# Kernel tuning notes

Hardware: AMD Instinct MI355X
Metric: run time of the kernel (lower is better)

Reference implementation:

```python
import jax, jax.numpy as jnp
import numpy as np

H, W, C_IN, C_OUT, N = 512, 512, 256, 256, 65536


def setup_inputs() -> dict:
    key = jax.random.key(0)
    k1, k2, k3, k4 = jax.random.split(key, 4)
    feature = jax.random.normal(k1, (1, C_IN, H, W), dtype=jnp.float32)
    weight = jax.random.normal(k2, (C_OUT, C_IN, 3, 3), dtype=jnp.float32) * 0.05
    # base sparse locations in the unpadded map; build 3x3 neighborhood indices
    # into the PADDED ([H+2, W+2]) map, exactly like F.pad + fancy indexing.
    base_h = jax.random.randint(k3, (N,), 0, H, dtype=jnp.int32)
    base_w = jax.random.randint(k4, (N,), 0, W, dtype=jnp.int32)
    dh = jnp.repeat(jnp.arange(3, dtype=jnp.int32), 3)  # [9]: 0,0,0,1,1,1,2,2,2
    dw = jnp.tile(jnp.arange(3, dtype=jnp.int32), 3)    # [9]: 0,1,2,0,1,2,...
    h_idx = base_h[None, :] + dh[:, None]  # [9, N], values in [0, H+1]
    w_idx = base_w[None, :] + dw[:, None]  # [9, N], values in [0, W+1]
    return {"feature": feature, "weight": weight, "h_idx": h_idx, "w_idx": w_idx}


def reference(feature, weight, h_idx, w_idx):
    # feature: [1, C, H, W]; weight: [Cout, C, 3, 3]; h_idx/w_idx: [9, N]
    C = feature.shape[1]
    out_ch = weight.shape[0]
    # F.pad(feature, [1,1,1,1])[0] -> [C, H+2, W+2]
    padded = jnp.pad(feature, ((0, 0), (0, 0), (1, 1), (1, 1)))[0]
    # gather 3x3 neighborhoods at sparse locations -> [C, 9, N]
    gathered = padded[:, h_idx, w_idx]
    # .view(9*C, -1): contiguous reshape gives row index c*9 + k
    g = gathered.reshape(C * 9, -1)  # [C*9, N]
    # kernel_d2s = weight.view(out, -1): row ordering c*9 + (kh*3+kw) matches
    k2d = weight.reshape(out_ch, -1)  # [Cout, C*9]
    return k2d @ g  # [Cout, N]
```

## Files before the change

### kernel.cpp

```cpp
#include <hip/hip_runtime.h>
#include <hip/hip_bf16.h>

#define HH 512
#define WW 512
#define CIN 256
#define COUT 256
#define NPTS 65536
#define PW 514
#define NPIX (PW * PW)
#define NKT 72

typedef __bf16 bf16x8 __attribute__((ext_vector_type(8)));
typedef float f32x16 __attribute__((ext_vector_type(16)));
typedef unsigned short us8 __attribute__((ext_vector_type(8)));

static __device__ __forceinline__ unsigned short f2bf(float f) {
  unsigned u = __builtin_bit_cast(unsigned, f);
  unsigned r = u + 0x7fffu + ((u >> 16) & 1u);
  return (unsigned short)(r >> 16);
}

static __device__ __forceinline__ void gload16(const void* g, void* l) {
  __builtin_amdgcn_global_load_lds(
      (const __attribute__((address_space(1))) unsigned int*)g,
      (__attribute__((address_space(3))) unsigned int*)l, 16, 0, 0);
}

__global__ __launch_bounds__(256) void prep_weight(const float* __restrict__ w,
                                                   unsigned short* __restrict__ A) {
  int i = blockIdx.x * 256 + threadIdx.x;
  int kt = i >> 13;
  int o  = i & 8191;
  int r  = o >> 5;
  int cp = (o >> 3) & 3;
  int j  = o & 7;
  int c  = cp ^ ((r >> 1) & 3);
  int k  = kt * 32 + c * 8 + j;
  int t  = k >> 8;
  int ci = k & 255;
  A[i] = f2bf(w[r * 2304 + ci * 9 + t]);
}

__global__ __launch_bounds__(256) void border_zero(unsigned short* __restrict__ Ft) {
  int g = blockIdx.x * 256 + threadIdx.x;
  if (g >= 2052 * 32) return;
  int p = g >> 5, c = g & 31;
  int py, px;
  if (p < 514)        { py = 0;        px = p; }
  else if (p < 1028)  { py = 513;      px = p - 514; }
  else if (p < 1540)  { py = p - 1027; px = 0; }
  else                { py = p - 1539; px = 513; }
  *(us8*)&Ft[((size_t)py * PW + px) * 256 + c * 8] = (us8){0, 0, 0, 0, 0, 0, 0, 0};
}

__global__ __launch_bounds__(256) void transpose_feat(const float* __restrict__ f,
                                                      unsigned short* __restrict__ Ft) {
  __shared__ unsigned short lds[64 * 264];
  int pix0 = blockIdx.x * 64;
  int y = pix0 >> 9, x0 = pix0 & 511;
  int tid = threadIdx.x;
  int p = tid & 63;
  int cb = tid >> 6;
  const float* src = f + pix0 + p;
  for (int c8 = 0; c8 < 8; ++c8) {
    us8 v;
#pragma unroll
    for (int j = 0; j < 8; ++j) {
      int ci = cb * 64 + c8 * 8 + j;
      v[j] = f2bf(src[ci * 262144]);
    }
    *(us8*)&lds[p * 264 + cb * 64 + c8 * 8] = v;
  }
  __syncthreads();
  int cic = tid & 31;
  int pr = tid >> 5;
  for (int g = 0; g < 8; ++g) {
    int p2 = pr + g * 8;
    us8 v = *(const us8*)&lds[p2 * 264 + cic * 8];
    *(us8*)&Ft[((size_t)((y + 1) * PW + x0 + 1 + p2)) * 256 + cic * 8] = v;
  }
}

__global__ __launch_bounds__(512, 2) void gemm_gather(
    const unsigned short* __restrict__ A,
    const unsigned short* __restrict__ Ft,
    const int* __restrict__ hidx,
    const int* __restrict__ widx,
    float* __restrict__ out) {
  __shared__ unsigned short lds[73728];
  unsigned short* ldsB = lds + 24576;

  int tid = threadIdx.x;
  int lane = tid & 63, wv = tid >> 6;
  int wm = wv & 1, wn = wv >> 1;
  int n0 = blockIdx.x << 8;

  int lcB = (tid & 7) ^ ((tid >> 3) & 7);
  const unsigned short* FtQ0;
  const unsigned short* FtQ1;
  const unsigned short* FtQ2;
  const unsigned short* FtQ3;
  {
    int cq = tid >> 3;
    FtQ0 = Ft + (long)(hidx[n0 + cq] * PW + widx[n0 + cq]) * 256 + lcB * 8;
    FtQ1 = Ft + (long)(hidx[n0 + 64 + cq] * PW + widx[n0 + 64 + cq]) * 256 + lcB * 8;
    FtQ2 = Ft + (long)(hidx[n0 + 128 + cq] * PW + widx[n0 + 128 + cq]) * 256 + lcB * 8;
    FtQ3 = Ft + (long)(hidx[n0 + 192 + cq] * PW + widx[n0 + 192 + cq]) * 256 + lcB * 8;
  }

#define STAGE_A(t_, ab_)                                                      \
  do {                                                                        \
    const unsigned short* g_ = A + (size_t)(t_) * 8192 + tid * 8;             \
    unsigned short* l_ = lds + (ab_) * 8192 + tid * 8;                        \
    gload16(g_, l_);                                                          \
    gload16(g_ + 4096, l_ + 4096);                                            \
  } while (0)

#define STAGE_B(p_, bb_)                                                      \
  do {                                                                        \
    int tap_ = (p_) >> 2;                                                     \
    long off_ = (long)((tap_ / 3) * PW + (tap_ - (tap_ / 3) * 3)) * 256 +     \
                ((p_) & 3) * 64;                                              \
    unsigned short* l_ = ldsB + (bb_) * 16384 + tid * 8;                      \
    gload16(FtQ0 + off_, l_);                                                 \
    gload16(FtQ1 + off_, l_ + 4096);                                          \
    gload16(FtQ2 + off_, l_ + 8192);                                          \
    gload16(FtQ3 + off_, l_ + 12288);                                         \
  } while (0)

#define LDA(dst, ab_, kg_, mt_)                                               \
  do {                                                                        \
    int r_ = wm * 128 + (mt_) * 32 + (lane & 31);                             \
    int c_ = ((kg_) * 2 + (lane >> 5)) ^ ((r_ >> 1) & 3);                     \
    dst = *(const bf16x8*)&lds[(ab_) * 8192 + r_ * 32 + c_ * 8];              \
  } while (0)

#define LDB(dst, bb_, s_, kg_, nt_)                                           \
  do {                                                                        \
    int col_ = wn * 64 + (nt_) * 32 + (lane & 31);                            \
    int pc_ = ((s_) * 4 + (kg_) * 2 + (lane >> 5)) ^ (col_ & 7);              \
    dst = *(const bf16x8*)&ldsB[(bb_) * 16384 + col_ * 64 + pc_ * 8];         \
  } while (0)

#define MFMA8(a0, a1, a2, a3, b0, b1)                                         \
  do {                                                                        \
    __builtin_amdgcn_s_setprio(1);                                            \
    acc[0][0] = __builtin_amdgcn_mfma_f32_32x32x16_bf16(a0, b0, acc[0][0], 0, 0, 0); \
    acc[0][1] = __builtin_amdgcn_mfma_f32_32x32x16_bf16(a0, b1, acc[0][1], 0, 0, 0); \
    acc[1][0] = __builtin_amdgcn_mfma_f32_32x32x16_bf16(a1, b0, acc[1][0], 0, 0, 0); \
    acc[1][1] = __builtin_amdgcn_mfma_f32_32x32x16_bf16(a1, b1, acc[1][1], 0, 0, 0); \
    acc[2][0] = __builtin_amdgcn_mfma_f32_32x32x16_bf16(a2, b0, acc[2][0], 0, 0, 0); \
    acc[2][1] = __builtin_amdgcn_mfma_f32_32x32x16_bf16(a2, b1, acc[2][1], 0, 0, 0); \
    acc[3][0] = __builtin_amdgcn_mfma_f32_32x32x16_bf16(a3, b0, acc[3][0], 0, 0, 0); \
    acc[3][1] = __builtin_amdgcn_mfma_f32_32x32x16_bf16(a3, b1, acc[3][1], 0, 0, 0); \
    __builtin_amdgcn_s_setprio(0);                                            \
  } while (0)

#define HEAD(W_)                                                              \
  do {                                                                        \
    asm volatile("s_waitcnt lgkmcnt(0)" ::: "memory");                        \
    asm volatile("s_waitcnt vmcnt(" #W_ ")" ::: "memory");                    \
    __builtin_amdgcn_s_barrier();                                             \
    __builtin_amdgcn_sched_barrier(0);                                        \
  } while (0)

#define TILE_BODY(ab_, bb_, s_)                                               \
  bf16x8 xa0, xa1, xa2, xa3, xb0, xb1, ya0, ya1, ya2, ya3, yb0, yb1;          \
  LDA(xa0, ab_, 0, 0); LDA(xa1, ab_, 0, 1); LDA(xa2, ab_, 0, 2);              \
  LDA(xa3, ab_, 0, 3); LDB(xb0, bb_, s_, 0, 0); LDB(xb1, bb_, s_, 0, 1)

#define TILE_TAIL(ab_, bb_, s_)                                               \
  LDA(ya0, ab_, 1, 0); LDA(ya1, ab_, 1, 1); LDA(ya2, ab_, 1, 2);              \
  LDA(ya3, ab_, 1, 3); LDB(yb0, bb_, s_, 1, 0); LDB(yb1, bb_, s_, 1, 1);      \
  MFMA8(xa0, xa1, xa2, xa3, xb0, xb1);                                        \
  MFMA8(ya0, ya1, ya2, ya3, yb0, yb1)

  f32x16 acc[4][2];
#pragma unroll
  for (int mt = 0; mt < 4; ++mt)
#pragma unroll
    for (int nt = 0; nt < 2; ++nt)
      acc[mt][nt] = (f32x16)(0.f);

  STAGE_A(0, 0);
  STAGE_B(0, 0);
  STAGE_A(1, 1);
  STAGE_B(1, 1);

  int abE = 0, bbP = 0;
  for (int p = 0; p < 34; ++p) {
    int abO = abE + 1; if (abO == 3) abO = 0;
    int abN = abO + 1; if (abN == 3) abN = 0;
    int bbN = bbP + 2; if (bbN >= 3) bbN -= 3;
    {
      HEAD(6);
      TILE_BODY(abE, bbP, 0);
      STAGE_A(2 * p + 2, abN);
      STAGE_B(p + 2, bbN);
      TILE_TAIL(abE, bbP, 0);
    }
    {
      HEAD(6);
      TILE_BODY(abO, bbP, 1);
      STAGE_A(2 * p + 3, abE);
      TILE_TAIL(abO, bbP, 1);
    }
    abE = abN;
    bbP = bbP + 1; if (bbP == 3) bbP = 0;
  }
  {
    HEAD(6);
    TILE_BODY(2, 1, 0);
    STAGE_A(70, 1);
    TILE_TAIL(2, 1, 0);
  }
  {
    HEAD(2);
    TILE_BODY(0, 1, 1);
    STAGE_A(71, 2);
    TILE_TAIL(0, 1, 1);
  }
  {
    HEAD(2);
    TILE_BODY(1, 2, 0);
    TILE_TAIL(1, 2, 0);
  }
  {
    HEAD(0);
    TILE_BODY(2, 2, 1);
    TILE_TAIL(2, 2, 1);
  }

#undef STAGE_A
#undef STAGE_B
#undef LDA
#undef LDB
#undef MFMA8
#undef HEAD
#undef TILE_BODY
#undef TILE_TAIL

  int colb = n0 + wn * 64 + (lane & 31);
  int rb = wm * 128 + ((lane >> 5) << 2);
#pragma unroll
  for (int mt = 0; mt < 4; ++mt)
#pragma unroll
    for (int nt = 0; nt < 2; ++nt)
#pragma unroll
      for (int r = 0; r < 16; ++r) {
        int row = rb + mt * 32 + (r & 3) + ((r >> 2) << 3);
        out[(size_t)row * NPTS + colb + nt * 32] = acc[mt][nt][r];
      }
}

__global__ __launch_bounds__(256) void naive_conv(const float* __restrict__ f,
                                                  const float* __restrict__ w,
                                                  const int* __restrict__ hi,
                                                  const int* __restrict__ wi,
                                                  float* __restrict__ out) {
  int idx = blockIdx.x * 256 + threadIdx.x;
  int n = idx & (NPTS - 1);
  int co = idx >> 16;
  int bh = hi[n] - 1;
  int bw = wi[n] - 1;
  float acc = 0.f;
  for (int ci = 0; ci < CIN; ++ci) {
    const float* fc = f + (size_t)ci * 262144;
    const float* wc = w + (size_t)co * 2304 + ci * 9;
#pragma unroll
    for (int t = 0; t < 9; ++t) {
      int y = bh + t / 3, x = bw + t % 3;
      float v = (y >= 0 && y < 512 && x >= 0 && x < 512) ? fc[y * 512 + x] : 0.f;
      acc += wc[t] * v;
    }
  }
  out[(size_t)co * NPTS + n] = acc;
}

extern "C" void kernel_launch(void* const* d_in, const int* in_sizes, int n_in,
                              void* d_out, int out_size, void* d_ws, size_t ws_size,
                              hipStream_t stream) {
  const float* feature = (const float*)d_in[0];
  const float* weight  = (const float*)d_in[1];
  const int* hidx      = (const int*)d_in[2];
  const int* widx      = (const int*)d_in[3];
  float* out           = (float*)d_out;

  const size_t FT_OFF = 2ull * 1024 * 1024;
  const size_t FT_BYTES = (size_t)NPIX * 256 * 2;
  const size_t NEED = FT_OFF + FT_BYTES;

  if (ws_size >= NEED) {
    unsigned short* Abf = (unsigned short*)d_ws;
    unsigned short* Ft = (unsigned short*)((char*)d_ws + FT_OFF);
    prep_weight<<<(NKT * 8192) / 256, 256, 0, stream>>>(weight, Abf);
    border_zero<<<(2052 * 32 + 255) / 256, 256, 0, stream>>>(Ft);
    transpose_feat<<<262144 / 64, 256, 0, stream>>>(feature, Ft);
    gemm_gather<<<NPTS / 256, 512, 0, stream>>>(Abf, Ft, hidx, widx, out);
  } else {
    naive_conv<<<(COUT * NPTS) / 256, 256, 0, stream>>>(feature, weight, hidx, widx, out);
  }
}
```

Baseline: 173.8 us.

## Restructure B gather to per-k-tile staging with deeper six-buffer prefetch

B tiles now hold 32 channels per k-tile instead of 64 channels covering two k-tiles. They are staged once per iteration into a six-deep ring, five tiles ahead, while A keeps its three-deep ring two tiles ahead. The main loop becomes a uniform unrolled 6-step body with a constant vmcnt wait and clamped tail prefetches, replacing the special-cased prologue and epilogue. This aims to keep more gather loads in flight to hide the latency of the random-access B gather. In exchange, each gather load is smaller and less contiguous, and the tail re-issues redundant loads.

```diff
diff --git a/kernel.cpp b/kernel.cpp
--- a/kernel.cpp
+++ b/kernel.cpp
@@ -95,17 +95,13 @@
   int wm = wv & 1, wn = wv >> 1;
   int n0 = blockIdx.x << 8;
 
-  int lcB = (tid & 7) ^ ((tid >> 3) & 7);
+  int lcB = (tid & 3) ^ ((tid >> 3) & 3);
   const unsigned short* FtQ0;
   const unsigned short* FtQ1;
-  const unsigned short* FtQ2;
-  const unsigned short* FtQ3;
   {
-    int cq = tid >> 3;
+    int cq = tid >> 2;
     FtQ0 = Ft + (long)(hidx[n0 + cq] * PW + widx[n0 + cq]) * 256 + lcB * 8;
-    FtQ1 = Ft + (long)(hidx[n0 + 64 + cq] * PW + widx[n0 + 64 + cq]) * 256 + lcB * 8;
-    FtQ2 = Ft + (long)(hidx[n0 + 128 + cq] * PW + widx[n0 + 128 + cq]) * 256 + lcB * 8;
-    FtQ3 = Ft + (long)(hidx[n0 + 192 + cq] * PW + widx[n0 + 192 + cq]) * 256 + lcB * 8;
+    FtQ1 = Ft + (long)(hidx[n0 + 128 + cq] * PW + widx[n0 + 128 + cq]) * 256 + lcB * 8;
   }
 
 #define STAGE_A(t_, ab_)                                                      \
@@ -116,16 +112,14 @@
     gload16(g_ + 4096, l_ + 4096);                                            \
   } while (0)
 
-#define STAGE_B(p_, bb_)                                                      \
-  do {                                                                        \
-    int tap_ = (p_) >> 2;                                                     \
+#define STAGE_B(t_, bb_)                                                      \
+  do {                                                                        \
+    int tap_ = (t_) >> 3;                                                     \
     long off_ = (long)((tap_ / 3) * PW + (tap_ - (tap_ / 3) * 3)) * 256 +     \
-                ((p_) & 3) * 64;                                              \
-    unsigned short* l_ = ldsB + (bb_) * 16384 + tid * 8;                      \
+                ((t_) & 7) * 32;                                              \
+    unsigned short* l_ = ldsB + (bb_) * 8192 + tid * 8;                       \
     gload16(FtQ0 + off_, l_);                                                 \
     gload16(FtQ1 + off_, l_ + 4096);                                          \
-    gload16(FtQ2 + off_, l_ + 8192);                                          \
-    gload16(FtQ3 + off_, l_ + 12288);                                         \
   } while (0)
 
 #define LDA(dst, ab_, kg_, mt_)                                               \
@@ -135,11 +129,11 @@
     dst = *(const bf16x8*)&lds[(ab_) * 8192 + r_ * 32 + c_ * 8];              \
   } while (0)
 
-#define LDB(dst, bb_, s_, kg_, nt_)                                           \
+#define LDB(dst, bb_, kg_, nt_)                                               \
   do {                                                                        \
     int col_ = wn * 64 + (nt_) * 32 + (lane & 31);                            \
-    int pc_ = ((s_) * 4 + (kg_) * 2 + (lane >> 5)) ^ (col_ & 7);              \
-    dst = *(const bf16x8*)&ldsB[(bb_) * 16384 + col_ * 64 + pc_ * 8];         \
+    int pc_ = ((kg_) * 2 + (lane >> 5)) ^ ((col_ >> 1) & 3);                  \
+    dst = *(const bf16x8*)&ldsB[(bb_) * 8192 + col_ * 32 + pc_ * 8];          \
   } while (0)
 
 #define MFMA8(a0, a1, a2, a3, b0, b1)                                         \
@@ -156,25 +150,14 @@
     __builtin_amdgcn_s_setprio(0);                                            \
   } while (0)
 
-#define HEAD(W_)                                                              \
+#define HEAD()                                                                \
   do {                                                                        \
     asm volatile("s_waitcnt lgkmcnt(0)" ::: "memory");                        \
-    asm volatile("s_waitcnt vmcnt(" #W_ ")" ::: "memory");                    \
+    asm volatile("s_waitcnt vmcnt(6)" ::: "memory");                          \
     __builtin_amdgcn_s_barrier();                                             \
     __builtin_amdgcn_sched_barrier(0);                                        \
   } while (0)
 
-#define TILE_BODY(ab_, bb_, s_)                                               \
-  bf16x8 xa0, xa1, xa2, xa3, xb0, xb1, ya0, ya1, ya2, ya3, yb0, yb1;          \
-  LDA(xa0, ab_, 0, 0); LDA(xa1, ab_, 0, 1); LDA(xa2, ab_, 0, 2);              \
-  LDA(xa3, ab_, 0, 3); LDB(xb0, bb_, s_, 0, 0); LDB(xb1, bb_, s_, 0, 1)
-
-#define TILE_TAIL(ab_, bb_, s_)                                               \
-  LDA(ya0, ab_, 1, 0); LDA(ya1, ab_, 1, 1); LDA(ya2, ab_, 1, 2);              \
-  LDA(ya3, ab_, 1, 3); LDB(yb0, bb_, s_, 1, 0); LDB(yb1, bb_, s_, 1, 1);      \
-  MFMA8(xa0, xa1, xa2, xa3, xb0, xb1);                                        \
-  MFMA8(ya0, ya1, ya2, ya3, yb0, yb1)
-
   f32x16 acc[4][2];
 #pragma unroll
   for (int mt = 0; mt < 4; ++mt)
@@ -182,53 +165,31 @@
     for (int nt = 0; nt < 2; ++nt)
       acc[mt][nt] = (f32x16)(0.f);
 
+  STAGE_B(0, 0);
+  STAGE_B(1, 1);
+  STAGE_B(2, 2);
   STAGE_A(0, 0);
-  STAGE_B(0, 0);
+  STAGE_B(3, 3);
   STAGE_A(1, 1);
-  STAGE_B(1, 1);
-
-  int abE = 0, bbP = 0;
-  for (int p = 0; p < 34; ++p) {
-    int abO = abE + 1; if (abO == 3) abO = 0;
-    int abN = abO + 1; if (abN == 3) abN = 0;
-    int bbN = bbP + 2; if (bbN >= 3) bbN -= 3;
-    {
-      HEAD(6);
-      TILE_BODY(abE, bbP, 0);
-      STAGE_A(2 * p + 2, abN);
-      STAGE_B(p + 2, bbN);
-      TILE_TAIL(abE, bbP, 0);
+  STAGE_B(4, 4);
+
+  for (int p = 0; p < 12; ++p) {
+#pragma unroll
+    for (int u = 0; u < 6; ++u) {
+      int t = p * 6 + u;
+      const int ab = u % 3;
+      const int bb = u;
+      HEAD();
+      bf16x8 xa0, xa1, xa2, xa3, xb0, xb1, ya0, ya1, ya2, ya3, yb0, yb1;
+      LDA(xa0, ab, 0, 0); LDA(xa1, ab, 0, 1); LDA(xa2, ab, 0, 2);
+      LDA(xa3, ab, 0, 3); LDB(xb0, bb, 0, 0); LDB(xb1, bb, 0, 1);
+      STAGE_A((t + 2 < NKT ? t + 2 : NKT - 1), (u + 2) % 3);
+      STAGE_B((t + 5 < NKT ? t + 5 : NKT - 1), (u + 5) % 6);
+      LDA(ya0, ab, 1, 0); LDA(ya1, ab, 1, 1); LDA(ya2, ab, 1, 2);
+      LDA(ya3, ab, 1, 3); LDB(yb0, bb, 1, 0); LDB(yb1, bb, 1, 1);
+      MFMA8(xa0, xa1, xa2, xa3, xb0, xb1);
+      MFMA8(ya0, ya1, ya2, ya3, yb0, yb1);
     }
-    {
-      HEAD(6);
-      TILE_BODY(abO, bbP, 1);
-      STAGE_A(2 * p + 3, abE);
-      TILE_TAIL(abO, bbP, 1);
-    }
-    abE = abN;
-    bbP = bbP + 1; if (bbP == 3) bbP = 0;
-  }
-  {
-    HEAD(6);
-    TILE_BODY(2, 1, 0);
-    STAGE_A(70, 1);
-    TILE_TAIL(2, 1, 0);
-  }
-  {
-    HEAD(2);
-    TILE_BODY(0, 1, 1);
-    STAGE_A(71, 2);
-    TILE_TAIL(0, 1, 1);
-  }
-  {
-    HEAD(2);
-    TILE_BODY(1, 2, 0);
-    TILE_TAIL(1, 2, 0);
-  }
-  {
-    HEAD(0);
-    TILE_BODY(2, 2, 1);
-    TILE_TAIL(2, 2, 1);
   }
 
 #undef STAGE_A
@@ -237,8 +198,6 @@
 #undef LDB
 #undef MFMA8
 #undef HEAD
-#undef TILE_BODY
-#undef TILE_TAIL
 
   int colb = n0 + wn * 64 + (lane & 31);
   int rb = wm * 128 + ((lane >> 5) << 2);
```

Result: no change. 176.8 us (+1.7%).
